# Performance work log

Measured on AMD Instinct MI355X. Metric: run time of the kernel, lower is better.

Reference implementation:

```python
import jax, jax.numpy as jnp
import numpy as np

# BitLinear (BitNet-style) constants, reconstructed from missing helpers:
#   get_qb_range(b) -> (-2^(b-1), 2^(b-1));  Qb = 2^(b-1) = 128 for bit_range=8
#   get_beta(W)  = mean(|W|)   (||W||_1 / (n*m))
#   get_gamma(W) = max(|W|)
QB = 128.0
EP = 0.01        # ep init arg: clip margin
LN_EPS = 1e-5    # nn.LayerNorm default eps
N_IN = 4096
N_OUT = 4096


def setup_inputs() -> dict:
    key = jax.random.key(0)
    kx, kw = jax.random.split(key, 2)
    x = jax.random.normal(kx, (4, 2048, N_IN), dtype=jnp.float32)
    # weight_init(): w0 ~ N(0,1); alpha = mean(w0); binarize sign(w0 - alpha)
    w0 = jax.random.normal(kw, (N_IN, N_OUT), dtype=jnp.float32)
    alpha = jnp.mean(w0)
    beta = jnp.mean(jnp.abs(w0))          # get_beta
    gamma = jnp.max(jnp.abs(w0))          # get_gamma
    w = jnp.where(w0 - alpha > 0, 1.0, -1.0).astype(jnp.float32)
    ln_gamma = jnp.ones((N_IN,), dtype=jnp.float32)   # LayerNorm weight
    ln_beta = jnp.zeros((N_IN,), dtype=jnp.float32)   # LayerNorm bias
    return {"x": x, "w": w, "ln_gamma": ln_gamma, "ln_beta": ln_beta,
            "beta": beta, "gamma": gamma}


def reference(x, w, ln_gamma, ln_beta, beta, gamma):
    # LayerNorm over last dim
    mu = jnp.mean(x, axis=-1, keepdims=True)
    var = jnp.mean(jnp.square(x - mu), axis=-1, keepdims=True)
    xn = (x - mu) * jax.lax.rsqrt(var + LN_EPS) * ln_gamma + ln_beta
    # ABSMax quantize: scale by Qb/gamma, clip to [-Qb+ep, Qb-ep] (no int cast)
    xq = jnp.clip(xn * (QB / gamma), -QB + EP, QB - EP)
    # binary-weight matmul + dequant scale beta*gamma/Qb
    y = jnp.einsum("bsi,io->bso", xq, w) * (beta * gamma / QB)
    return y
```

## Files before the change

kernel.cpp:

```cpp
#include <hip/hip_runtime.h>

using f32x4  = __attribute__((ext_vector_type(4))) float;
using i32x4  = __attribute__((ext_vector_type(4))) int;
using i32x16 = __attribute__((ext_vector_type(16))) int;

constexpr int K_DIM = 4096;
constexpr int N_DIM = 4096;
constexpr float QBf = 128.0f;
constexpr float EPf = 0.01f;
constexpr float LN_EPSf = 1e-5f;

#define GLOAD_LDS16(gp, lp)                                                  \
    __builtin_amdgcn_global_load_lds(                                        \
        (const __attribute__((address_space(1))) void*)(gp),                 \
        (__attribute__((address_space(3))) void*)(lp), 16, 0, 0)

#define BARRIER()                                                            \
    do { asm volatile("" ::: "memory");                                      \
         __builtin_amdgcn_s_barrier();                                       \
         asm volatile("" ::: "memory"); } while (0)

#define WAIT_LGKM(N)                                                         \
    do { asm volatile("s_waitcnt lgkmcnt(" #N ")" ::: "memory");             \
         __builtin_amdgcn_sched_barrier(0); } while (0)

__global__ __launch_bounds__(256) void ln_quant_kernel(
    const float* __restrict__ x,
    const float* __restrict__ ln_g,
    const float* __restrict__ ln_b,
    const float* __restrict__ gamma_p,
    char* __restrict__ xq)
{
    const int row = blockIdx.x;
    const int t = threadIdx.x;
    const float4* xr4 = reinterpret_cast<const float4*>(x + (size_t)row * K_DIM);

    float4 v[4];
    float sum = 0.f, sumsq = 0.f;
#pragma unroll
    for (int i = 0; i < 4; ++i) {
        v[i] = xr4[t * 4 + i];
        sum += v[i].x + v[i].y + v[i].z + v[i].w;
        sumsq += v[i].x * v[i].x + v[i].y * v[i].y + v[i].z * v[i].z + v[i].w * v[i].w;
    }
#pragma unroll
    for (int off = 32; off > 0; off >>= 1) {
        sum += __shfl_down(sum, off);
        sumsq += __shfl_down(sumsq, off);
    }
    __shared__ float s_sum[4], s_sq[4];
    const int lane = t & 63, w = t >> 6;
    if (lane == 0) { s_sum[w] = sum; s_sq[w] = sumsq; }
    __syncthreads();
    sum = s_sum[0] + s_sum[1] + s_sum[2] + s_sum[3];
    sumsq = s_sq[0] + s_sq[1] + s_sq[2] + s_sq[3];

    const float mu = sum * (1.0f / K_DIM);
    const float var = sumsq * (1.0f / K_DIM) - mu * mu;
    const float rstd = rsqrtf(var + LN_EPSf);
    const float qs = QBf / gamma_p[0];
    const float lo = -QBf + EPf, hi = QBf - EPf;

    alignas(16) char ob[16];
#pragma unroll
    for (int i = 0; i < 4; ++i) {
        const float4 g = reinterpret_cast<const float4*>(ln_g)[t * 4 + i];
        const float4 b = reinterpret_cast<const float4*>(ln_b)[t * 4 + i];
        const float f0 = fminf(fmaxf(((v[i].x - mu) * rstd * g.x + b.x) * qs, lo), hi);
        const float f1 = fminf(fmaxf(((v[i].y - mu) * rstd * g.y + b.y) * qs, lo), hi);
        const float f2 = fminf(fmaxf(((v[i].z - mu) * rstd * g.z + b.z) * qs, lo), hi);
        const float f3 = fminf(fmaxf(((v[i].w - mu) * rstd * g.w + b.w) * qs, lo), hi);
        int x0 = (int)rintf(f0), x1 = (int)rintf(f1);
        int x2 = (int)rintf(f2), x3 = (int)rintf(f3);
        ob[i * 4 + 0] = (char)(x0 > 127 ? 127 : x0);
        ob[i * 4 + 1] = (char)(x1 > 127 ? 127 : x1);
        ob[i * 4 + 2] = (char)(x2 > 127 ? 127 : x2);
        ob[i * 4 + 3] = (char)(x3 > 127 ? 127 : x3);
    }
    *reinterpret_cast<uint4*>(xq + (size_t)row * K_DIM + t * 16) =
        *reinterpret_cast<const uint4*>(ob);
}

__global__ __launch_bounds__(256) void wtrans_kernel(
    const float* __restrict__ w, char* __restrict__ wq)
{
    __shared__ char tile[64][68];
    const int t = threadIdx.x;
    const int bk = blockIdx.y * 64;
    const int bn = blockIdx.x * 64;
#pragma unroll
    for (int i = 0; i < 4; ++i) {
        const int li = i * 1024 + t * 4;
        const int r = li >> 6, c = li & 63;
        const float4 vv = *reinterpret_cast<const float4*>(
            w + (size_t)(bk + r) * N_DIM + bn + c);
        tile[r][c]     = (char)vv.x;
        tile[r][c + 1] = (char)vv.y;
        tile[r][c + 2] = (char)vv.z;
        tile[r][c + 3] = (char)vv.w;
    }
    __syncthreads();
    const int n = t >> 2, kc = t & 3;
    alignas(16) char h16[16];
#pragma unroll
    for (int j = 0; j < 16; ++j) h16[j] = tile[kc * 16 + j][n];
    *reinterpret_cast<uint4*>(wq + (size_t)(bn + n) * K_DIM + bk + kc * 16) =
        *reinterpret_cast<const uint4*>(h16);
}

__global__ __launch_bounds__(512, 2) void gemm_kernel(
    const char* __restrict__ A,
    const char* __restrict__ Bt,
    float* __restrict__ C,
    const float* __restrict__ beta_p,
    const float* __restrict__ gamma_p)
{
    constexpr int NT = K_DIM / 64;
    __shared__ __align__(16) char lds[131072];

    const int t = threadIdx.x;
    const int flat = blockIdx.y * gridDim.x + blockIdx.x;
    const int xcd = flat & 7;
    const int r8 = flat >> 3;
    const int by = ((xcd >> 1) << 3) + (r8 >> 3);
    const int bx = ((xcd & 1) << 3) + (r8 & 7);
    const int bm = by * 256;
    const int bn = bx * 256;

    const int lane = t & 63;
    const int w = t >> 6;
    const int wm = w >> 2;
    const int wn = w & 3;
    const int ln31 = lane & 31;
    const int lg2 = lane >> 5;

    const char* gA = A + (size_t)bm * K_DIM;
    const char* gB = Bt + (size_t)bn * K_DIM;
    const int voff = (t & 127) * K_DIM + (t >> 7) * 16;

    const int aoff = lg2 * 2048 + ln31 * 16;
    const int boff = lg2 * 2048 + ((wn & 1) * 64 + ln31) * 16;

#define STAGE_HT(b, ht, kt)                                                   \
    GLOAD_LDS16((((ht) < 2) ? gA : gB)                                        \
                    + (size_t)(((ht) & 1) * (128 * K_DIM) + (kt) * 64) + voff,\
                lds + (b) * 32768 + (((ht) < 2) ? 0 : 16384)                  \
                    + ((ht) & 1) * 8192 + t * 16)

#define READ_A(par, ks, mfp)                                                  \
    do {                                                                      \
        afr[par][0] = *reinterpret_cast<const i32x4*>(                        \
            abase + (ks) * 4096 + ((mfp) * 2) * 512 + aoff);                  \
        afr[par][1] = *reinterpret_cast<const i32x4*>(                        \
            abase + (ks) * 4096 + ((mfp) * 2 + 1) * 512 + aoff);              \
    } while (0)

#define MFMA4(par, ks, mfp)                                                   \
    do {                                                                      \
        __builtin_amdgcn_s_setprio(1);                                        \
        _Pragma("unroll")                                                     \
        for (int m2 = 0; m2 < 2; ++m2)                                        \
            _Pragma("unroll")                                                 \
            for (int nf = 0; nf < 2; ++nf)                                    \
                acc[(mfp) * 2 + m2][nf] =                                     \
                    __builtin_amdgcn_mfma_i32_32x32x32_i8(                    \
                        afr[par][m2], bfrag[nf][ks],                          \
                        acc[(mfp) * 2 + m2][nf], 0, 0, 0);                    \
        __builtin_amdgcn_s_setprio(0);                                        \
    } while (0)

    i32x16 acc[4][2];
#pragma unroll
    for (int m = 0; m < 4; ++m)
#pragma unroll
        for (int n = 0; n < 2; ++n)
#pragma unroll
            for (int q = 0; q < 16; ++q)
                acc[m][n][q] = 0;

    STAGE_HT(0, 0, 0); STAGE_HT(0, 1, 0); STAGE_HT(0, 2, 0); STAGE_HT(0, 3, 0);
    STAGE_HT(1, 0, 1); STAGE_HT(1, 1, 1); STAGE_HT(1, 2, 1); STAGE_HT(1, 3, 1);
    STAGE_HT(2, 0, 2); STAGE_HT(2, 1, 2); STAGE_HT(2, 2, 2); STAGE_HT(2, 3, 2);
    asm volatile("s_waitcnt vmcnt(8)" ::: "memory");
    BARRIER();

    for (int kt = 0; kt < NT; kt += 4) {
#pragma unroll
        for (int h = 0; h < 4; ++h) {
            const int tt = kt + h;
            const int sb = (h + 3) & 3;
            const char* abase = lds + h * 32768 + wm * 8192;
            const char* bbase = lds + h * 32768 + 16384 + (wn >> 1) * 8192;

            i32x4 bfrag[2][2];
            i32x4 afr[2][2];

#pragma unroll
            for (int nf = 0; nf < 2; ++nf)
#pragma unroll
                for (int ks = 0; ks < 2; ++ks)
                    bfrag[nf][ks] = *reinterpret_cast<const i32x4*>(
                        bbase + ks * 4096 + nf * 512 + boff);
            READ_A(0, 0, 0);

            READ_A(1, 0, 1);
            if (tt + 3 < NT) { STAGE_HT(sb, 0, tt + 3); STAGE_HT(sb, 1, tt + 3); }
            WAIT_LGKM(2);
            MFMA4(0, 0, 0);

            READ_A(0, 1, 0);
            WAIT_LGKM(2);
            MFMA4(1, 0, 1);

            READ_A(1, 1, 1);
            if (tt + 3 < NT) { STAGE_HT(sb, 2, tt + 3); STAGE_HT(sb, 3, tt + 3); }
            WAIT_LGKM(2);
            MFMA4(0, 1, 0);

            WAIT_LGKM(0);
            MFMA4(1, 1, 1);
            asm volatile("s_waitcnt vmcnt(8)" ::: "memory");
            BARRIER();
        }
    }

    const float scale = beta_p[0] * gamma_p[0] * (1.0f / QBf);
    const int orow0 = bm + wm * 128 + lg2 * 4;
    const int ocol0 = bn + wn * 64 + ln31;
#pragma unroll
    for (int mf = 0; mf < 4; ++mf) {
#pragma unroll
        for (int nf = 0; nf < 2; ++nf) {
#pragma unroll
            for (int reg = 0; reg < 16; ++reg) {
                const int row = orow0 + mf * 32 + (reg & 3) + 8 * (reg >> 2);
                C[(size_t)row * N_DIM + ocol0 + nf * 32] =
                    (float)acc[mf][nf][reg] * scale;
            }
        }
    }
#undef STAGE_HT
#undef READ_A
#undef MFMA4
}

extern "C" void kernel_launch(void* const* d_in, const int* in_sizes, int n_in,
                              void* d_out, int out_size, void* d_ws, size_t ws_size,
                              hipStream_t stream)
{
    const float* x       = (const float*)d_in[0];
    const float* w       = (const float*)d_in[1];
    const float* ln_g    = (const float*)d_in[2];
    const float* ln_b    = (const float*)d_in[3];
    const float* beta_p  = (const float*)d_in[4];
    const float* gamma_p = (const float*)d_in[5];
    float* out = (float*)d_out;

    const int M = in_sizes[0] / K_DIM;

    char* xq = (char*)d_ws;
    char* wq = (char*)d_ws + (size_t)M * K_DIM;

    ln_quant_kernel<<<M, 256, 0, stream>>>(x, ln_g, ln_b, gamma_p, xq);
    wtrans_kernel<<<dim3(N_DIM / 64, K_DIM / 64), 256, 0, stream>>>(w, wq);
    gemm_kernel<<<dim3(N_DIM / 256, M / 256), 512, 0, stream>>>(xq, wq, out, beta_p, gamma_p);
}
```

Baseline: 248.8 us.

## Use 1024-thread GEMM blocks with 64x64 per-wave tiles and triple buffering

The int8 GEMM block grows from 8 to 16 waves while keeping the 256x256 output tile, so each wave now computes a 64x64 sub-tile with 2x2 MFMAs instead of 128x64. The LDS pipeline shrinks from four 32KB stages to three, and each stage is now loaded by a single A and a single B global-to-LDS load per thread. The intent is more resident waves per CU to hide latency, with lower register pressure. The cost is more LDS fragment reads per MFMA and one less stage of prefetch depth.

After: 334.5 us. 1.34x slower.

```diff
diff --git a/kernel.cpp b/kernel.cpp
--- a/kernel.cpp
+++ b/kernel.cpp
@@ -1,6 +1,5 @@
 #include <hip/hip_runtime.h>
 
-using f32x4  = __attribute__((ext_vector_type(4))) float;
 using i32x4  = __attribute__((ext_vector_type(4))) int;
 using i32x16 = __attribute__((ext_vector_type(16))) int;
 
@@ -23,6 +22,8 @@
 #define WAIT_LGKM(N)                                                         \
     do { asm volatile("s_waitcnt lgkmcnt(" #N ")" ::: "memory");             \
          __builtin_amdgcn_sched_barrier(0); } while (0)
+
+#define FENCE() __builtin_amdgcn_sched_barrier(0)
 
 __global__ __launch_bounds__(256) void ln_quant_kernel(
     const float* __restrict__ x,
@@ -108,7 +109,7 @@
         *reinterpret_cast<const uint4*>(h16);
 }
 
-__global__ __launch_bounds__(512, 2) void gemm_kernel(
+__global__ __launch_bounds__(1024, 4) void gemm_kernel(
     const char* __restrict__ A,
     const char* __restrict__ Bt,
     float* __restrict__ C,
@@ -116,7 +117,7 @@
     const float* __restrict__ gamma_p)
 {
     constexpr int NT = K_DIM / 64;
-    __shared__ __align__(16) char lds[131072];
+    __shared__ __align__(16) char lds[98304];
 
     const int t = threadIdx.x;
     const int flat = blockIdx.y * gridDim.x + blockIdx.x;
@@ -136,99 +137,82 @@
 
     const char* gA = A + (size_t)bm * K_DIM;
     const char* gB = Bt + (size_t)bn * K_DIM;
-    const int voff = (t & 127) * K_DIM + (t >> 7) * 16;
-
-    const int aoff = lg2 * 2048 + ln31 * 16;
-    const int boff = lg2 * 2048 + ((wn & 1) * 64 + ln31) * 16;
-
-#define STAGE_HT(b, ht, kt)                                                   \
-    GLOAD_LDS16((((ht) < 2) ? gA : gB)                                        \
-                    + (size_t)(((ht) & 1) * (128 * K_DIM) + (kt) * 64) + voff,\
-                lds + (b) * 32768 + (((ht) < 2) ? 0 : 16384)                  \
-                    + ((ht) & 1) * 8192 + t * 16)
-
-#define READ_A(par, ks, mfp)                                                  \
+    const int voff = (t & 255) * K_DIM + (t >> 8) * 16;
+
+    const int aoff = lg2 * 4096 + ((wm * 64 + ln31) << 4);
+    const int boff = lg2 * 4096 + ((wn * 64 + ln31) << 4);
+
+#define STAGE_AB(b, kt)                                                       \
     do {                                                                      \
-        afr[par][0] = *reinterpret_cast<const i32x4*>(                        \
-            abase + (ks) * 4096 + ((mfp) * 2) * 512 + aoff);                  \
-        afr[par][1] = *reinterpret_cast<const i32x4*>(                        \
-            abase + (ks) * 4096 + ((mfp) * 2 + 1) * 512 + aoff);              \
+        GLOAD_LDS16(gA + (size_t)(kt) * 64 + voff,                            \
+                    lds + (b) * 32768 + t * 16);                              \
+        GLOAD_LDS16(gB + (size_t)(kt) * 64 + voff,                            \
+                    lds + (b) * 32768 + 16384 + t * 16);                      \
     } while (0)
 
-#define MFMA4(par, ks, mfp)                                                   \
+#define LD(p) (*reinterpret_cast<const i32x4*>(p))
+
+#define MFMA4(ks)                                                             \
     do {                                                                      \
         __builtin_amdgcn_s_setprio(1);                                        \
         _Pragma("unroll")                                                     \
-        for (int m2 = 0; m2 < 2; ++m2)                                        \
+        for (int mf = 0; mf < 2; ++mf)                                        \
             _Pragma("unroll")                                                 \
             for (int nf = 0; nf < 2; ++nf)                                    \
-                acc[(mfp) * 2 + m2][nf] =                                     \
-                    __builtin_amdgcn_mfma_i32_32x32x32_i8(                    \
-                        afr[par][m2], bfrag[nf][ks],                          \
-                        acc[(mfp) * 2 + m2][nf], 0, 0, 0);                    \
+                acc[mf][nf] = __builtin_amdgcn_mfma_i32_32x32x32_i8(          \
+                    afr[ks][mf], bfr[ks][nf], acc[mf][nf], 0, 0, 0);          \
         __builtin_amdgcn_s_setprio(0);                                        \
     } while (0)
 
-    i32x16 acc[4][2];
-#pragma unroll
-    for (int m = 0; m < 4; ++m)
+#define TILE(b, sb, tt)                                                       \
+    do {                                                                      \
+        const char* ab = lds + (b) * 32768;                                   \
+        const char* bb = ab + 16384;                                          \
+        i32x4 afr[2][2], bfr[2][2];                           \
+        bfr[0][0] = LD(bb + boff);                                            \
+        bfr[0][1] = LD(bb + boff + 512);                                      \
+        afr[0][0] = LD(ab + aoff);                                            \
+        afr[0][1] = LD(ab + aoff + 512);                                      \
+        FENCE();                                                              \
+        bfr[1][0] = LD(bb + boff + 8192);                                     \
+        bfr[1][1] = LD(bb + boff + 8192 + 512);                               \
+        afr[1][0] = LD(ab + aoff + 8192);                                     \
+        afr[1][1] = LD(ab + aoff + 8192 + 512);                               \
+        if ((tt) + 2 < NT) STAGE_AB(sb, (tt) + 2);                            \
+        WAIT_LGKM(4);                                                         \
+        MFMA4(0);                                                             \
+        WAIT_LGKM(0);                                                         \
+        MFMA4(1);                                                             \
+        if ((tt) + 2 < NT) asm volatile("s_waitcnt vmcnt(2)" ::: "memory");   \
+        else               asm volatile("s_waitcnt vmcnt(0)" ::: "memory");   \
+        BARRIER();                                                            \
+    } while (0)
+
+    i32x16 acc[2][2];
+#pragma unroll
+    for (int m = 0; m < 2; ++m)
 #pragma unroll
         for (int n = 0; n < 2; ++n)
 #pragma unroll
             for (int q = 0; q < 16; ++q)
                 acc[m][n][q] = 0;
 
-    STAGE_HT(0, 0, 0); STAGE_HT(0, 1, 0); STAGE_HT(0, 2, 0); STAGE_HT(0, 3, 0);
-    STAGE_HT(1, 0, 1); STAGE_HT(1, 1, 1); STAGE_HT(1, 2, 1); STAGE_HT(1, 3, 1);
-    STAGE_HT(2, 0, 2); STAGE_HT(2, 1, 2); STAGE_HT(2, 2, 2); STAGE_HT(2, 3, 2);
-    asm volatile("s_waitcnt vmcnt(8)" ::: "memory");
+    STAGE_AB(0, 0); STAGE_AB(1, 1);
+    asm volatile("s_waitcnt vmcnt(2)" ::: "memory");
     BARRIER();
 
-    for (int kt = 0; kt < NT; kt += 4) {
-#pragma unroll
-        for (int h = 0; h < 4; ++h) {
-            const int tt = kt + h;
-            const int sb = (h + 3) & 3;
-            const char* abase = lds + h * 32768 + wm * 8192;
-            const char* bbase = lds + h * 32768 + 16384 + (wn >> 1) * 8192;
-
-            i32x4 bfrag[2][2];
-            i32x4 afr[2][2];
-
-#pragma unroll
-            for (int nf = 0; nf < 2; ++nf)
-#pragma unroll
-                for (int ks = 0; ks < 2; ++ks)
-                    bfrag[nf][ks] = *reinterpret_cast<const i32x4*>(
-                        bbase + ks * 4096 + nf * 512 + boff);
-            READ_A(0, 0, 0);
-
-            READ_A(1, 0, 1);
-            if (tt + 3 < NT) { STAGE_HT(sb, 0, tt + 3); STAGE_HT(sb, 1, tt + 3); }
-            WAIT_LGKM(2);
-            MFMA4(0, 0, 0);
-
-            READ_A(0, 1, 0);
-            WAIT_LGKM(2);
-            MFMA4(1, 0, 1);
-
-            READ_A(1, 1, 1);
-            if (tt + 3 < NT) { STAGE_HT(sb, 2, tt + 3); STAGE_HT(sb, 3, tt + 3); }
-            WAIT_LGKM(2);
-            MFMA4(0, 1, 0);
-
-            WAIT_LGKM(0);
-            MFMA4(1, 1, 1);
-            asm volatile("s_waitcnt vmcnt(8)" ::: "memory");
-            BARRIER();
-        }
-    }
+    for (int kt = 0; kt < NT - 1; kt += 3) {
+        TILE(0, 2, kt);
+        TILE(1, 0, kt + 1);
+        TILE(2, 1, kt + 2);
+    }
+    TILE(0, 2, NT - 1);
 
     const float scale = beta_p[0] * gamma_p[0] * (1.0f / QBf);
-    const int orow0 = bm + wm * 128 + lg2 * 4;
+    const int orow0 = bm + wm * 64 + lg2 * 4;
     const int ocol0 = bn + wn * 64 + ln31;
 #pragma unroll
-    for (int mf = 0; mf < 4; ++mf) {
+    for (int mf = 0; mf < 2; ++mf) {
 #pragma unroll
         for (int nf = 0; nf < 2; ++nf) {
 #pragma unroll
@@ -239,9 +223,10 @@
             }
         }
     }
-#undef STAGE_HT
-#undef READ_A
+#undef STAGE_AB
+#undef LD
 #undef MFMA4
+#undef TILE
 }
 
 extern "C" void kernel_launch(void* const* d_in, const int* in_sizes, int n_in,
@@ -263,5 +248,5 @@
 
     ln_quant_kernel<<<M, 256, 0, stream>>>(x, ln_g, ln_b, gamma_p, xq);
     wtrans_kernel<<<dim3(N_DIM / 64, K_DIM / 64), 256, 0, stream>>>(w, wq);
-    gemm_kernel<<<dim3(N_DIM / 256, M / 256), 512, 0, stream>>>(xq, wq, out, beta_p, gamma_p);
-}
+    gemm_kernel<<<dim3(N_DIM / 256, M / 256), 1024, 0, stream>>>(xq, wq, out, beta_p, gamma_p);
+}
```

## Switch GEMM to K=128 tiles with staggered A/B double-buffer prefetch

Applied to the files above, without the earlier changes.

The int8 GEMM main loop now works on K-steps of 128 instead of 64, so there are half as many iterations and barriers per tile pass. The four 32 KB LDS stages are replaced by two 64 KB buffers. A and B are prefetched on different schedules: A for the next tile goes into the other buffer, and B for tile+2 goes into the current buffer after a mid-tile barrier. This cuts barrier and wait overhead per unit of MFMA work, but the shallower prefetch distance may expose more global-load latency.

Result: faster. 218.7 us (-12.1%).

```diff
diff --git a/kernel.cpp b/kernel.cpp
--- a/kernel.cpp
+++ b/kernel.cpp
@@ -1,6 +1,5 @@
 #include <hip/hip_runtime.h>
 
-using f32x4  = __attribute__((ext_vector_type(4))) float;
 using i32x4  = __attribute__((ext_vector_type(4))) int;
 using i32x16 = __attribute__((ext_vector_type(16))) int;
 
@@ -23,6 +22,8 @@
 #define WAIT_LGKM(N)                                                         \
     do { asm volatile("s_waitcnt lgkmcnt(" #N ")" ::: "memory");             \
          __builtin_amdgcn_sched_barrier(0); } while (0)
+
+#define FENCE() __builtin_amdgcn_sched_barrier(0)
 
 __global__ __launch_bounds__(256) void ln_quant_kernel(
     const float* __restrict__ x,
@@ -115,7 +116,7 @@
     const float* __restrict__ beta_p,
     const float* __restrict__ gamma_p)
 {
-    constexpr int NT = K_DIM / 64;
+    constexpr int NT = K_DIM / 128;
     __shared__ __align__(16) char lds[131072];
 
     const int t = threadIdx.x;
@@ -136,23 +137,34 @@
 
     const char* gA = A + (size_t)bm * K_DIM;
     const char* gB = Bt + (size_t)bn * K_DIM;
-    const int voff = (t & 127) * K_DIM + (t >> 7) * 16;
-
-    const int aoff = lg2 * 2048 + ln31 * 16;
-    const int boff = lg2 * 2048 + ((wn & 1) * 64 + ln31) * 16;
-
-#define STAGE_HT(b, ht, kt)                                                   \
-    GLOAD_LDS16((((ht) < 2) ? gA : gB)                                        \
-                    + (size_t)(((ht) & 1) * (128 * K_DIM) + (kt) * 64) + voff,\
-                lds + (b) * 32768 + (((ht) < 2) ? 0 : 16384)                  \
-                    + ((ht) & 1) * 8192 + t * 16)
+    const int voff = (t & 127) * K_DIM + ((t >> 7) << 4);
+
+    const int aoff = lg2 * 2048 + (ln31 << 4);
+    const int boff = lg2 * 2048 + (((wn & 1) * 64 + ln31) << 4);
+
+#define STAGE_OP(gbase, b, roff, kt)                                          \
+    do {                                                                      \
+        GLOAD_LDS16((gbase) + (size_t)(kt) * 128 + voff,                      \
+                    lds + (b) * 65536 + (roff) + t * 16);                     \
+        GLOAD_LDS16((gbase) + (size_t)(kt) * 128 + voff + 64,                 \
+                    lds + (b) * 65536 + (roff) + 8192 + t * 16);              \
+        GLOAD_LDS16((gbase) + (size_t)(128 * K_DIM) + (size_t)(kt) * 128      \
+                        + voff,                                               \
+                    lds + (b) * 65536 + (roff) + 16384 + t * 16);             \
+        GLOAD_LDS16((gbase) + (size_t)(128 * K_DIM) + (size_t)(kt) * 128      \
+                        + voff + 64,                                          \
+                    lds + (b) * 65536 + (roff) + 16384 + 8192 + t * 16);      \
+    } while (0)
+
+#define STAGE_A(b, kt) STAGE_OP(gA, b, 0, kt)
+#define STAGE_B(b, kt) STAGE_OP(gB, b, 32768, kt)
+
+#define LD(p) (*reinterpret_cast<const i32x4*>(p))
 
 #define READ_A(par, ks, mfp)                                                  \
     do {                                                                      \
-        afr[par][0] = *reinterpret_cast<const i32x4*>(                        \
-            abase + (ks) * 4096 + ((mfp) * 2) * 512 + aoff);                  \
-        afr[par][1] = *reinterpret_cast<const i32x4*>(                        \
-            abase + (ks) * 4096 + ((mfp) * 2 + 1) * 512 + aoff);              \
+        afr[par][0] = LD(ab + (ks) * 4096 + (mfp) * 1024 + aoff);             \
+        afr[par][1] = LD(ab + (ks) * 4096 + (mfp) * 1024 + 512 + aoff);       \
     } while (0)
 
 #define MFMA4(par, ks, mfp)                                                   \
@@ -169,6 +181,37 @@
         __builtin_amdgcn_s_setprio(0);                                        \
     } while (0)
 
+#define TILE(b, tt)                                                           \
+    do {                                                                      \
+        const char* ab = lds + (b) * 65536 + wm * 16384;                      \
+        const char* bb = lds + (b) * 65536 + 32768 + (wn >> 1) * 16384;       \
+        i32x4 bfrag[2][4];                                      \
+        i32x4 afr[2][2];                                    \
+        _Pragma("unroll")                                                     \
+        for (int nf = 0; nf < 2; ++nf)                                        \
+            _Pragma("unroll")                                                 \
+            for (int ks = 0; ks < 4; ++ks)                                    \
+                bfrag[nf][ks] = LD(bb + ks * 4096 + nf * 512 + boff);         \
+        READ_A(0, 0, 0);                                                      \
+        FENCE();                                                              \
+         READ_A(1, 0, 1);                                             \
+        if ((tt) + 1 < NT) STAGE_A((b) ^ 1, (tt) + 1);                        \
+        WAIT_LGKM(2); MFMA4(0, 0, 0);                                         \
+         READ_A(0, 1, 0); WAIT_LGKM(2); MFMA4(1, 0, 1);               \
+         READ_A(1, 1, 1); WAIT_LGKM(2); MFMA4(0, 1, 0);               \
+         READ_A(0, 2, 0); WAIT_LGKM(2); MFMA4(1, 1, 1);               \
+        BARRIER();                                                            \
+         READ_A(1, 2, 1);                                             \
+        if ((tt) + 2 < NT) STAGE_B(b, (tt) + 2);                              \
+        WAIT_LGKM(2); MFMA4(0, 2, 0);                                         \
+         READ_A(0, 3, 0); WAIT_LGKM(2); MFMA4(1, 2, 1);               \
+         READ_A(1, 3, 1); WAIT_LGKM(2); MFMA4(0, 3, 0);               \
+         WAIT_LGKM(0); MFMA4(1, 3, 1);                                \
+        if ((tt) + 2 < NT) asm volatile("s_waitcnt vmcnt(4)" ::: "memory");   \
+        else               asm volatile("s_waitcnt vmcnt(0)" ::: "memory");   \
+        BARRIER();                                                            \
+    } while (0)
+
     i32x16 acc[4][2];
 #pragma unroll
     for (int m = 0; m < 4; ++m)
@@ -178,50 +221,13 @@
             for (int q = 0; q < 16; ++q)
                 acc[m][n][q] = 0;
 
-    STAGE_HT(0, 0, 0); STAGE_HT(0, 1, 0); STAGE_HT(0, 2, 0); STAGE_HT(0, 3, 0);
-    STAGE_HT(1, 0, 1); STAGE_HT(1, 1, 1); STAGE_HT(1, 2, 1); STAGE_HT(1, 3, 1);
-    STAGE_HT(2, 0, 2); STAGE_HT(2, 1, 2); STAGE_HT(2, 2, 2); STAGE_HT(2, 3, 2);
-    asm volatile("s_waitcnt vmcnt(8)" ::: "memory");
+    STAGE_A(0, 0); STAGE_B(0, 0); STAGE_B(1, 1);
+    asm volatile("s_waitcnt vmcnt(4)" ::: "memory");
     BARRIER();
 
-    for (int kt = 0; kt < NT; kt += 4) {
-#pragma unroll
-        for (int h = 0; h < 4; ++h) {
-            const int tt = kt + h;
-            const int sb = (h + 3) & 3;
-            const char* abase = lds + h * 32768 + wm * 8192;
-            const char* bbase = lds + h * 32768 + 16384 + (wn >> 1) * 8192;
-
-            i32x4 bfrag[2][2];
-            i32x4 afr[2][2];
-
-#pragma unroll
-            for (int nf = 0; nf < 2; ++nf)
-#pragma unroll
-                for (int ks = 0; ks < 2; ++ks)
-                    bfrag[nf][ks] = *reinterpret_cast<const i32x4*>(
-                        bbase + ks * 4096 + nf * 512 + boff);
-            READ_A(0, 0, 0);
-
-            READ_A(1, 0, 1);
-            if (tt + 3 < NT) { STAGE_HT(sb, 0, tt + 3); STAGE_HT(sb, 1, tt + 3); }
-            WAIT_LGKM(2);
-            MFMA4(0, 0, 0);
-
-            READ_A(0, 1, 0);
-            WAIT_LGKM(2);
-            MFMA4(1, 0, 1);
-
-            READ_A(1, 1, 1);
-            if (tt + 3 < NT) { STAGE_HT(sb, 2, tt + 3); STAGE_HT(sb, 3, tt + 3); }
-            WAIT_LGKM(2);
-            MFMA4(0, 1, 0);
-
-            WAIT_LGKM(0);
-            MFMA4(1, 1, 1);
-            asm volatile("s_waitcnt vmcnt(8)" ::: "memory");
-            BARRIER();
-        }
+    for (int kt = 0; kt < NT; kt += 2) {
+        TILE(0, kt);
+        TILE(1, kt + 1);
     }
 
     const float scale = beta_p[0] * gamma_p[0] * (1.0f / QBf);
@@ -239,9 +245,13 @@
             }
         }
     }
-#undef STAGE_HT
+#undef STAGE_OP
+#undef STAGE_A
+#undef STAGE_B
+#undef LD
 #undef READ_A
 #undef MFMA4
+#undef TILE
 }
 
 extern "C" void kernel_launch(void* const* d_in, const int* in_sizes, int n_in,
```
